# Kernel tuning notes

Measured on AMD Instinct MI355X. Metric: run time of the kernel, lower is better.

The kernel has to match this reference:

```python
import jax, jax.numpy as jnp
import numpy as np

N = 50000
E = 600000
D = 128
BN_EPS = 1e-5


def _gcn_layer(x, src, dst, ew, W, b, n):
    # x: [N, Din] -> [N, Dout]; PyG GCNConv: linear, symmetric norm (self-loops
    # already appended to src/dst/ew by caller), gather, scatter-add, bias.
    h = x @ W  # [N, Dout]
    deg = jax.ops.segment_sum(ew, dst, num_segments=n)  # [N]
    dinv = jnp.where(deg > 0, jax.lax.rsqrt(jnp.maximum(deg, 1e-30)), 0.0)
    norm = dinv[src] * ew * dinv[dst]  # [E+N]
    msg = h[src] * norm[:, None]  # [E+N, Dout] -- dominant memory traffic
    out = jax.ops.segment_sum(msg, dst, num_segments=n)
    return out + b


def _bn_eval(x, gamma, beta, mean, var):
    return (x - mean) * jax.lax.rsqrt(var + BN_EPS) * gamma + beta


def setup_inputs() -> dict:
    key = jax.random.key(0)
    ks = jax.random.split(key, 16)
    s = 1.0 / np.sqrt(D)
    inp = {
        "x": jax.random.normal(ks[0], (N, D), dtype=jnp.float32),
        "edge_index": jax.random.randint(ks[1], (2, E), 0, N, dtype=jnp.int32),
        "edge_weight": jax.random.uniform(ks[2], (E,), dtype=jnp.float32),
        "W0": jax.random.uniform(ks[3], (D, D), jnp.float32, -s, s),
        "b0": jnp.zeros((D,), jnp.float32),
        "W1": jax.random.uniform(ks[4], (D, D), jnp.float32, -s, s),
        "b1": jnp.zeros((D,), jnp.float32),
        "gamma0": jnp.ones((D,), jnp.float32),
        "beta0": jnp.zeros((D,), jnp.float32),
        "mean0": 0.1 * jax.random.normal(ks[5], (D,), jnp.float32),
        "var0": jax.random.uniform(ks[6], (D,), jnp.float32, 0.5, 1.5),
        "gamma1": jnp.ones((D,), jnp.float32),
        "beta1": jnp.zeros((D,), jnp.float32),
        "mean1": 0.1 * jax.random.normal(ks[7], (D,), jnp.float32),
        "var1": jax.random.uniform(ks[8], (D,), jnp.float32, 0.5, 1.5),
        "act_params": jnp.ones((2,), jnp.float32),  # activation_params init = ones(num_layers)
    }
    return inp


def reference(x, edge_index, edge_weight, W0, b0, W1, b1, gamma0, beta0, mean0, var0, gamma1, beta1, mean1, var1, act_params):
    # Add self-loops with weight 1 (PyG gcn_norm fill_value=1), shared by both layers.
    loop = jnp.arange(N, dtype=edge_index.dtype)
    src = jnp.concatenate([edge_index[0], loop])
    dst = jnp.concatenate([edge_index[1], loop])
    ew = jnp.concatenate([edge_weight, jnp.ones((N,), edge_weight.dtype)])

    # layer 0: conv -> BN (eval: running stats) -> adaptive ReLU/GELU blend
    h = _gcn_layer(x, src, dst, ew, W0, b0, N)
    h = _bn_eval(h, gamma0, beta0, mean0, var0)
    alpha = jax.nn.sigmoid(act_params[0])
    h = alpha * jax.nn.relu(h) + (1.0 - alpha) * jax.nn.gelu(h, approximate=False)
    # dropout: identity in eval mode

    # layer 1 (last): conv -> BN, no activation/dropout
    h = _gcn_layer(h, src, dst, ew, W1, b1, N)
    h = _bn_eval(h, gamma1, beta1, mean1, var1)
    return h
```

## Files before the change

kernel.cpp:

```cpp
#include <hip/hip_runtime.h>
#include <hip/hip_fp16.h>
#include <math.h>
#include <type_traits>

#define D 128
#define BN_EPS 1e-5f

typedef _Float16 half8 __attribute__((ext_vector_type(8)));
typedef float f32x4 __attribute__((ext_vector_type(4)));

__global__ void k_zero4(uint4* p, int n4) {
  int i = blockIdx.x * blockDim.x + threadIdx.x;
  if (i < n4) p[i] = make_uint4(0u, 0u, 0u, 0u);
}

__global__ void k_cnt_rank(const int* __restrict__ dst, int* cnt16,
                           int* __restrict__ rank, int e) {
  int i = blockIdx.x * blockDim.x + threadIdx.x;
  if (i < e) rank[i] = atomicAdd(&cnt16[(size_t)dst[i] * 16], 1);
}

__global__ __launch_bounds__(1024) void k_scan1(const int* __restrict__ cnt16,
                                                int* __restrict__ off, int* bsum, int n) {
  __shared__ int ws[16];
  const int tid = threadIdx.x;
  const int i = blockIdx.x * 1024 + tid;
  int v = (i < n) ? cnt16[(size_t)i * 16] : 0;
  int x = v;
#pragma unroll
  for (int d = 1; d < 64; d <<= 1) {
    int y = __shfl_up(x, d, 64);
    if ((tid & 63) >= d) x += y;
  }
  const int wid = tid >> 6;
  if ((tid & 63) == 63) ws[wid] = x;
  __syncthreads();
  if (wid == 0) {
    int s = (tid < 16) ? ws[tid] : 0;
#pragma unroll
    for (int d = 1; d < 16; d <<= 1) {
      int y = __shfl_up(s, d, 64);
      if (tid >= d && tid < 16) s += y;
    }
    if (tid < 16) ws[tid] = s;
  }
  __syncthreads();
  int woff = (wid > 0) ? ws[wid - 1] : 0;
  if (i < n) off[i] = woff + x - v;
  if (tid == 1023) bsum[blockIdx.x] = ws[15];
}

__global__ __launch_bounds__(1024) void k_scan2(int* bsum, int nb, int* total_loc) {
  __shared__ int ws[16];
  const int tid = threadIdx.x;
  int v = (tid < nb) ? bsum[tid] : 0;
  int x = v;
#pragma unroll
  for (int d = 1; d < 64; d <<= 1) {
    int y = __shfl_up(x, d, 64);
    if ((tid & 63) >= d) x += y;
  }
  const int wid = tid >> 6;
  if ((tid & 63) == 63) ws[wid] = x;
  __syncthreads();
  if (wid == 0) {
    int s = (tid < 16) ? ws[tid] : 0;
#pragma unroll
    for (int d = 1; d < 16; d <<= 1) {
      int y = __shfl_up(s, d, 64);
      if (tid >= d && tid < 16) s += y;
    }
    if (tid < 16) ws[tid] = s;
  }
  __syncthreads();
  int woff = (wid > 0) ? ws[wid - 1] : 0;
  if (tid < nb) bsum[tid] = woff + x - v;
  if (tid == 1023) *total_loc = ws[15];
}

__global__ __launch_bounds__(1024) void k_scan3(int* off, const int* __restrict__ bsum, int n) {
  const int i = blockIdx.x * 1024 + threadIdx.x;
  if (i < n) off[i] += bsum[blockIdx.x];
}

__global__ void k_bucket(const int* __restrict__ src, const int* __restrict__ dst,
                         const float* __restrict__ ew, const int* __restrict__ off,
                         const int* __restrict__ rank, uint2* __restrict__ pack, int e) {
  int i = blockIdx.x * blockDim.x + threadIdx.x;
  if (i < e) {
    int d = dst[i];
    int pos = off[d] + rank[i];
    pack[pos] = make_uint2((unsigned)src[i], __float_as_uint(ew[i]));
  }
}

__global__ void k_degdinv(const int* __restrict__ off, const uint2* __restrict__ pack,
                          float* __restrict__ dinv, int n) {
  int g = blockIdx.x * blockDim.x + threadIdx.x;
  if (g < n) {
    float deg = 1.0f;
    int k1 = off[g + 1];
    for (int k = off[g]; k < k1; ++k) deg += __uint_as_float(pack[k].y);
    dinv[g] = rsqrtf(deg);
  }
}

__global__ void k_packW(const float* __restrict__ W0, const float* __restrict__ W1,
                        _Float16* __restrict__ p0, _Float16* __restrict__ p1) {
  const float* W = blockIdx.x ? W1 : W0;
  _Float16* P = blockIdx.x ? p1 : p0;
  for (int idx = threadIdx.x; idx < 32 * 64; idx += 256) {
    int ntks = idx >> 6;
    int lane = idx & 63;
    int nt = ntks >> 2, ks = ntks & 3;
    int kb = ks * 32 + (lane >> 4) * 8;
    int c = nt * 16 + (lane & 15);
#pragma unroll
    for (int i = 0; i < 8; ++i)
      P[(size_t)idx * 8 + i] = (_Float16)W[(size_t)(kb + i) * D + c];
  }
}

template <typename T>
__global__ __launch_bounds__(256) void k_gemm_mfma(const T* __restrict__ X,
                                                   const _Float16* __restrict__ Bp,
                                                   __half* __restrict__ H, int n) {
  const int lane = threadIdx.x & 63;
  const int wave = threadIdx.x >> 6;
  const int r0 = blockIdx.x * 64 + wave * 16;
  const int arow = r0 + (lane & 15);
  const int kbase = (lane >> 4) * 8;
  const bool av = arow < n;

  f32x4 acc[8];
#pragma unroll
  for (int t = 0; t < 8; ++t) acc[t] = (f32x4){0.f, 0.f, 0.f, 0.f};

#pragma unroll
  for (int ks = 0; ks < 4; ++ks) {
    half8 a;
    if (av) {
      if constexpr (std::is_same<T, float>::value) {
        const float* ap = X + (size_t)arow * D + ks * 32 + kbase;
        float4 f0 = *(const float4*)ap;
        float4 f1 = *(const float4*)(ap + 4);
        a[0] = (_Float16)f0.x; a[1] = (_Float16)f0.y;
        a[2] = (_Float16)f0.z; a[3] = (_Float16)f0.w;
        a[4] = (_Float16)f1.x; a[5] = (_Float16)f1.y;
        a[6] = (_Float16)f1.z; a[7] = (_Float16)f1.w;
      } else {
        a = *(const half8*)((const __half*)X + (size_t)arow * D + ks * 32 + kbase);
      }
    } else {
#pragma unroll
      for (int i = 0; i < 8; ++i) a[i] = (_Float16)0.f;
    }
#pragma unroll
    for (int nt = 0; nt < 8; ++nt) {
      half8 b = *(const half8*)(Bp + ((size_t)(nt * 4 + ks) * 64 + lane) * 8);
      acc[nt] = __builtin_amdgcn_mfma_f32_16x16x32_f16(a, b, acc[nt], 0, 0, 0);
    }
  }

  const int rbase = (lane >> 4) * 4;
  const int col = lane & 15;
#pragma unroll
  for (int nt = 0; nt < 8; ++nt) {
#pragma unroll
    for (int j = 0; j < 4; ++j) {
      int rr = r0 + rbase + j;
      if (rr < n) H[(size_t)rr * D + nt * 16 + col] = __float2half(acc[nt][j]);
    }
  }
}

__device__ __forceinline__ void h8_to_f(const uint4& r, float* f) {
  const __half2* hp = (const __half2*)&r;
#pragma unroll
  for (int t = 0; t < 4; ++t) {
    float2 v = __half22float2(hp[t]);
    f[2 * t] = v.x; f[2 * t + 1] = v.y;
  }
}

template <typename OutT, bool ACT>
__global__ __launch_bounds__(256) void k_agg(const __half* __restrict__ H,
                                             const int* __restrict__ off,
                                             const uint2* __restrict__ pack,
                                             const float* __restrict__ dinv,
                                             const float* __restrict__ bias,
                                             const float* __restrict__ gamma,
                                             const float* __restrict__ beta,
                                             const float* __restrict__ mean,
                                             const float* __restrict__ var,
                                             const float* __restrict__ act_params,
                                             OutT* __restrict__ out, int n) {
  int g = blockIdx.x * 16 + (threadIdx.x >> 4);
  if (g >= n) return;
  const int j = (threadIdx.x & 15) * 8;

  float acc[8];
#pragma unroll
  for (int t = 0; t < 8; ++t) acc[t] = 0.f;

  int k = off[g], k1 = off[g + 1];
  for (; k + 3 < k1; k += 4) {
    uint2 p0 = pack[k], p1 = pack[k + 1], p2 = pack[k + 2], p3 = pack[k + 3];
    float w0 = dinv[p0.x] * __uint_as_float(p0.y);
    float w1 = dinv[p1.x] * __uint_as_float(p1.y);
    float w2 = dinv[p2.x] * __uint_as_float(p2.y);
    float w3 = dinv[p3.x] * __uint_as_float(p3.y);
    uint4 r0 = *(const uint4*)(H + (size_t)p0.x * D + j);
    uint4 r1 = *(const uint4*)(H + (size_t)p1.x * D + j);
    uint4 r2 = *(const uint4*)(H + (size_t)p2.x * D + j);
    uint4 r3 = *(const uint4*)(H + (size_t)p3.x * D + j);
    float f0[8], f1[8], f2[8], f3[8];
    h8_to_f(r0, f0); h8_to_f(r1, f1); h8_to_f(r2, f2); h8_to_f(r3, f3);
#pragma unroll
    for (int t = 0; t < 8; ++t)
      acc[t] += w0 * f0[t] + w1 * f1[t] + w2 * f2[t] + w3 * f3[t];
  }
  for (; k < k1; ++k) {
    uint2 p = pack[k];
    float w = dinv[p.x] * __uint_as_float(p.y);
    uint4 r = *(const uint4*)(H + (size_t)p.x * D + j);
    float f[8];
    h8_to_f(r, f);
#pragma unroll
    for (int t = 0; t < 8; ++t) acc[t] += w * f[t];
  }

  float dg = dinv[g];
  uint4 rs = *(const uint4*)(H + (size_t)g * D + j);
  float fs[8];
  h8_to_f(rs, fs);
#pragma unroll
  for (int t = 0; t < 8; ++t) acc[t] = dg * acc[t] + dg * dg * fs[t];

  float bb[8], gm[8], bt[8], mn[8], vr[8];
  *(float4*)&bb[0] = *(const float4*)(bias + j);  *(float4*)&bb[4] = *(const float4*)(bias + j + 4);
  *(float4*)&gm[0] = *(const float4*)(gamma + j); *(float4*)&gm[4] = *(const float4*)(gamma + j + 4);
  *(float4*)&bt[0] = *(const float4*)(beta + j);  *(float4*)&bt[4] = *(const float4*)(beta + j + 4);
  *(float4*)&mn[0] = *(const float4*)(mean + j);  *(float4*)&mn[4] = *(const float4*)(mean + j + 4);
  *(float4*)&vr[0] = *(const float4*)(var + j);   *(float4*)&vr[4] = *(const float4*)(var + j + 4);

  float alpha = ACT ? 1.f / (1.f + expf(-act_params[0])) : 0.f;

#pragma unroll
  for (int t = 0; t < 8; ++t) {
    float vv = (acc[t] + bb[t] - mn[t]) * rsqrtf(vr[t] + BN_EPS) * gm[t] + bt[t];
    if (ACT) {
      float rl = fmaxf(vv, 0.f);
      float ge = 0.5f * vv * (1.f + erff(vv * 0.70710678118654752f));
      vv = alpha * rl + (1.f - alpha) * ge;
    }
    acc[t] = vv;
  }
  if constexpr (std::is_same<OutT, __half>::value) {
    uint4 st;
    __half2* hp = (__half2*)&st;
    hp[0] = __floats2half2_rn(acc[0], acc[1]);
    hp[1] = __floats2half2_rn(acc[2], acc[3]);
    hp[2] = __floats2half2_rn(acc[4], acc[5]);
    hp[3] = __floats2half2_rn(acc[6], acc[7]);
    *(uint4*)(out + (size_t)g * D + j) = st;
  } else {
    *(float4*)(out + (size_t)g * D + j)     = make_float4(acc[0], acc[1], acc[2], acc[3]);
    *(float4*)(out + (size_t)g * D + j + 4) = make_float4(acc[4], acc[5], acc[6], acc[7]);
  }
}

extern "C" void kernel_launch(void* const* d_in, const int* in_sizes, int n_in,
                              void* d_out, int out_size, void* d_ws, size_t ws_size,
                              hipStream_t stream) {
  const float* x      = (const float*)d_in[0];
  const int*   ei     = (const int*)d_in[1];
  const float* ew     = (const float*)d_in[2];
  const float* W0     = (const float*)d_in[3];
  const float* b0     = (const float*)d_in[4];
  const float* W1     = (const float*)d_in[5];
  const float* b1     = (const float*)d_in[6];
  const float* gamma0 = (const float*)d_in[7];
  const float* beta0  = (const float*)d_in[8];
  const float* mean0  = (const float*)d_in[9];
  const float* var0   = (const float*)d_in[10];
  const float* gamma1 = (const float*)d_in[11];
  const float* beta1  = (const float*)d_in[12];
  const float* mean1  = (const float*)d_in[13];
  const float* var1   = (const float*)d_in[14];
  const float* act    = (const float*)d_in[15];

  const int n = in_sizes[0] / D;
  const int e = in_sizes[2];
  const int* srcp = ei;
  const int* dstp = ei + e;

  uintptr_t p = (uintptr_t)d_ws;
  auto carve = [&p](size_t bytes) -> void* {
    void* r = (void*)p;
    p += (bytes + 255) & ~(size_t)255;
    return r;
  };
  float*    dinv  = (float*)carve(sizeof(float) * n);
  int*      off   = (int*)carve(sizeof(int) * (n + 1));
  int*      rank  = (int*)carve(sizeof(int) * e);
  int*      bsum  = (int*)carve(sizeof(int) * 1024);
  int*      cnt16 = (int*)carve(sizeof(int) * (size_t)n * 16);
  _Float16* w0p   = (_Float16*)carve(sizeof(_Float16) * 32 * 64 * 8);
  _Float16* w1p   = (_Float16*)carve(sizeof(_Float16) * 32 * 64 * 8);
  uint2*    pack  = (uint2*)carve(sizeof(uint2) * e);
  __half*   h16   = (__half*)carve(sizeof(__half) * (size_t)n * D);
  __half*   a16   = (__half*)carve(sizeof(__half) * (size_t)n * D);
  float*    out   = (float*)d_out;

  const int tpb = 256;
  const int nb_n = (n + tpb - 1) / tpb;
  const int nb_e = (e + tpb - 1) / tpb;
  const int nb_s = (n + 1023) / 1024;
  const int Gg   = (n + 63) / 64;
  const int nz4  = n * 4;

  k_zero4<<<(nz4 + tpb - 1) / tpb, tpb, 0, stream>>>((uint4*)cnt16, nz4);
  k_packW<<<2, tpb, 0, stream>>>(W0, W1, w0p, w1p);
  k_cnt_rank<<<nb_e, tpb, 0, stream>>>(dstp, cnt16, rank, e);
  k_scan1<<<nb_s, 1024, 0, stream>>>(cnt16, off, bsum, n);
  k_scan2<<<1, 1024, 0, stream>>>(bsum, nb_s, off + n);
  k_scan3<<<nb_s, 1024, 0, stream>>>(off, bsum, n);
  k_bucket<<<nb_e, tpb, 0, stream>>>(srcp, dstp, ew, off, rank, pack, e);
  k_degdinv<<<nb_n, tpb, 0, stream>>>(off, pack, dinv, n);

  k_gemm_mfma<float><<<Gg, tpb, 0, stream>>>(x, w0p, h16, n);
  k_agg<__half, true><<<(n + 15) / 16, tpb, 0, stream>>>(
      h16, off, pack, dinv, b0, gamma0, beta0, mean0, var0, act, a16, n);

  k_gemm_mfma<__half><<<Gg, tpb, 0, stream>>>(a16, w1p, h16, n);
  k_agg<float, false><<<(n + 15) / 16, tpb, 0, stream>>>(
      h16, off, pack, dinv, b1, gamma1, beta1, mean1, var1, act, out, n);
}
```

Before: 146.1 us.

## Fuse preprocessing kernels and layer-0 aggregation with layer-1 GEMM

Merges zeroing and weight packing into one launch, and runs the edge-count atomics in the same launch as the first GEMM using block-index partitioning. The two scan tail kernels become one, with each block re-scanning the block sums in a single wavefront. The layer-0 aggregation now writes its activated rows into shared memory and immediately multiplies them by W1 with MFMA. This removes the intermediate half-precision activation buffer round trip and several kernel launches. The trade-offs are more shared memory per block, a block barrier inside the aggregation, and a scan that assumes at most 64 scan blocks.

```diff
diff --git a/kernel.cpp b/kernel.cpp
--- a/kernel.cpp
+++ b/kernel.cpp
@@ -9,15 +9,87 @@
 typedef _Float16 half8 __attribute__((ext_vector_type(8)));
 typedef float f32x4 __attribute__((ext_vector_type(4)));
 
-__global__ void k_zero4(uint4* p, int n4) {
-  int i = blockIdx.x * blockDim.x + threadIdx.x;
-  if (i < n4) p[i] = make_uint4(0u, 0u, 0u, 0u);
-}
-
-__global__ void k_cnt_rank(const int* __restrict__ dst, int* cnt16,
-                           int* __restrict__ rank, int e) {
-  int i = blockIdx.x * blockDim.x + threadIdx.x;
-  if (i < e) rank[i] = atomicAdd(&cnt16[(size_t)dst[i] * 16], 1);
+__global__ void k_init(uint4* __restrict__ z, int n4,
+                       const float* __restrict__ W0, const float* __restrict__ W1,
+                       _Float16* __restrict__ p0, _Float16* __restrict__ p1, int Z) {
+  if ((int)blockIdx.x < Z) {
+    int i = blockIdx.x * 256 + threadIdx.x;
+    if (i < n4) z[i] = make_uint4(0u, 0u, 0u, 0u);
+    return;
+  }
+  const float* W = (blockIdx.x - Z) ? W1 : W0;
+  _Float16* P = (blockIdx.x - Z) ? p1 : p0;
+  for (int idx = threadIdx.x; idx < 32 * 64; idx += 256) {
+    int ntks = idx >> 6;
+    int lane = idx & 63;
+    int nt = ntks >> 2, ks = ntks & 3;
+    int kb = ks * 32 + (lane >> 4) * 8;
+    int c = nt * 16 + (lane & 15);
+#pragma unroll
+    for (int i = 0; i < 8; ++i)
+      P[(size_t)idx * 8 + i] = (_Float16)W[(size_t)(kb + i) * D + c];
+  }
+}
+
+__global__ __launch_bounds__(256) void k_cnt_gemm0(const float* __restrict__ X,
+                                                   const _Float16* __restrict__ Bp,
+                                                   __half* __restrict__ H,
+                                                   const int* __restrict__ dst,
+                                                   int* cnt16, int* __restrict__ rank,
+                                                   int n, int e, int Gc) {
+  if ((int)blockIdx.x < Gc) {
+    int base = blockIdx.x * 1024 + threadIdx.x;
+#pragma unroll
+    for (int jj = 0; jj < 4; ++jj) {
+      int i = base + jj * 256;
+      if (i < e) rank[i] = atomicAdd(&cnt16[(size_t)dst[i] * 16], 1);
+    }
+    return;
+  }
+
+  const int lane = threadIdx.x & 63;
+  const int wave = threadIdx.x >> 6;
+  const int r0 = (blockIdx.x - Gc) * 64 + wave * 16;
+  const int arow = r0 + (lane & 15);
+  const int kbase = (lane >> 4) * 8;
+  const bool av = arow < n;
+
+  f32x4 acc[8];
+#pragma unroll
+  for (int t = 0; t < 8; ++t) acc[t] = (f32x4){0.f, 0.f, 0.f, 0.f};
+
+#pragma unroll
+  for (int ks = 0; ks < 4; ++ks) {
+    half8 a;
+    if (av) {
+      const float* ap = X + (size_t)arow * D + ks * 32 + kbase;
+      float4 f0 = *(const float4*)ap;
+      float4 f1 = *(const float4*)(ap + 4);
+      a[0] = (_Float16)f0.x; a[1] = (_Float16)f0.y;
+      a[2] = (_Float16)f0.z; a[3] = (_Float16)f0.w;
+      a[4] = (_Float16)f1.x; a[5] = (_Float16)f1.y;
+      a[6] = (_Float16)f1.z; a[7] = (_Float16)f1.w;
+    } else {
+#pragma unroll
+      for (int i = 0; i < 8; ++i) a[i] = (_Float16)0.f;
+    }
+#pragma unroll
+    for (int nt = 0; nt < 8; ++nt) {
+      half8 b = *(const half8*)(Bp + ((size_t)(nt * 4 + ks) * 64 + lane) * 8);
+      acc[nt] = __builtin_amdgcn_mfma_f32_16x16x32_f16(a, b, acc[nt], 0, 0, 0);
+    }
+  }
+
+  const int rbase = (lane >> 4) * 4;
+  const int col = lane & 15;
+#pragma unroll
+  for (int nt = 0; nt < 8; ++nt) {
+#pragma unroll
+    for (int j = 0; j < 4; ++j) {
+      int rr = r0 + rbase + j;
+      if (rr < n) H[(size_t)rr * D + nt * 16 + col] = __float2half(acc[nt][j]);
+    }
+  }
 }
 
 __global__ __launch_bounds__(1024) void k_scan1(const int* __restrict__ cnt16,
@@ -50,37 +122,25 @@
   if (tid == 1023) bsum[blockIdx.x] = ws[15];
 }
 
-__global__ __launch_bounds__(1024) void k_scan2(int* bsum, int nb, int* total_loc) {
-  __shared__ int ws[16];
+__global__ __launch_bounds__(1024) void k_scan23(int* off, const int* __restrict__ bsum,
+                                                 int n, int nb) {
+  __shared__ int sh[2];
   const int tid = threadIdx.x;
-  int v = (tid < nb) ? bsum[tid] : 0;
-  int x = v;
-#pragma unroll
-  for (int d = 1; d < 64; d <<= 1) {
-    int y = __shfl_up(x, d, 64);
-    if ((tid & 63) >= d) x += y;
-  }
-  const int wid = tid >> 6;
-  if ((tid & 63) == 63) ws[wid] = x;
+  if (tid < 64) {
+    int x = (tid < nb) ? bsum[tid] : 0;
+#pragma unroll
+    for (int d = 1; d < 64; d <<= 1) {
+      int y = __shfl_up(x, d, 64);
+      if (tid >= d) x += y;
+    }
+    int pfx = (blockIdx.x > 0) ? __shfl(x, (int)blockIdx.x - 1, 64) : 0;
+    int tot = __shfl(x, nb - 1, 64);
+    if (tid == 0) { sh[0] = pfx; sh[1] = tot; }
+  }
   __syncthreads();
-  if (wid == 0) {
-    int s = (tid < 16) ? ws[tid] : 0;
-#pragma unroll
-    for (int d = 1; d < 16; d <<= 1) {
-      int y = __shfl_up(s, d, 64);
-      if (tid >= d && tid < 16) s += y;
-    }
-    if (tid < 16) ws[tid] = s;
-  }
-  __syncthreads();
-  int woff = (wid > 0) ? ws[wid - 1] : 0;
-  if (tid < nb) bsum[tid] = woff + x - v;
-  if (tid == 1023) *total_loc = ws[15];
-}
-
-__global__ __launch_bounds__(1024) void k_scan3(int* off, const int* __restrict__ bsum, int n) {
-  const int i = blockIdx.x * 1024 + threadIdx.x;
-  if (i < n) off[i] += bsum[blockIdx.x];
+  const int i = blockIdx.x * 1024 + tid;
+  if (i < n) off[i] += sh[0];
+  if (blockIdx.x == 0 && tid == 0) off[n] = sh[1];
 }
 
 __global__ void k_bucket(const int* __restrict__ src, const int* __restrict__ dst,
@@ -105,81 +165,149 @@
   }
 }
 
-__global__ void k_packW(const float* __restrict__ W0, const float* __restrict__ W1,
-                        _Float16* __restrict__ p0, _Float16* __restrict__ p1) {
-  const float* W = blockIdx.x ? W1 : W0;
-  _Float16* P = blockIdx.x ? p1 : p0;
-  for (int idx = threadIdx.x; idx < 32 * 64; idx += 256) {
-    int ntks = idx >> 6;
-    int lane = idx & 63;
-    int nt = ntks >> 2, ks = ntks & 3;
-    int kb = ks * 32 + (lane >> 4) * 8;
-    int c = nt * 16 + (lane & 15);
-#pragma unroll
-    for (int i = 0; i < 8; ++i)
-      P[(size_t)idx * 8 + i] = (_Float16)W[(size_t)(kb + i) * D + c];
-  }
-}
-
-template <typename T>
-__global__ __launch_bounds__(256) void k_gemm_mfma(const T* __restrict__ X,
-                                                   const _Float16* __restrict__ Bp,
-                                                   __half* __restrict__ H, int n) {
-  const int lane = threadIdx.x & 63;
-  const int wave = threadIdx.x >> 6;
-  const int r0 = blockIdx.x * 64 + wave * 16;
-  const int arow = r0 + (lane & 15);
-  const int kbase = (lane >> 4) * 8;
-  const bool av = arow < n;
-
-  f32x4 acc[8];
-#pragma unroll
-  for (int t = 0; t < 8; ++t) acc[t] = (f32x4){0.f, 0.f, 0.f, 0.f};
-
-#pragma unroll
-  for (int ks = 0; ks < 4; ++ks) {
-    half8 a;
-    if (av) {
-      if constexpr (std::is_same<T, float>::value) {
-        const float* ap = X + (size_t)arow * D + ks * 32 + kbase;
-        float4 f0 = *(const float4*)ap;
-        float4 f1 = *(const float4*)(ap + 4);
-        a[0] = (_Float16)f0.x; a[1] = (_Float16)f0.y;
-        a[2] = (_Float16)f0.z; a[3] = (_Float16)f0.w;
-        a[4] = (_Float16)f1.x; a[5] = (_Float16)f1.y;
-        a[6] = (_Float16)f1.z; a[7] = (_Float16)f1.w;
-      } else {
-        a = *(const half8*)((const __half*)X + (size_t)arow * D + ks * 32 + kbase);
-      }
-    } else {
-#pragma unroll
-      for (int i = 0; i < 8; ++i) a[i] = (_Float16)0.f;
-    }
-#pragma unroll
-    for (int nt = 0; nt < 8; ++nt) {
-      half8 b = *(const half8*)(Bp + ((size_t)(nt * 4 + ks) * 64 + lane) * 8);
-      acc[nt] = __builtin_amdgcn_mfma_f32_16x16x32_f16(a, b, acc[nt], 0, 0, 0);
-    }
-  }
-
-  const int rbase = (lane >> 4) * 4;
-  const int col = lane & 15;
-#pragma unroll
-  for (int nt = 0; nt < 8; ++nt) {
-#pragma unroll
-    for (int j = 0; j < 4; ++j) {
-      int rr = r0 + rbase + j;
-      if (rr < n) H[(size_t)rr * D + nt * 16 + col] = __float2half(acc[nt][j]);
-    }
-  }
-}
-
 __device__ __forceinline__ void h8_to_f(const uint4& r, float* f) {
   const __half2* hp = (const __half2*)&r;
 #pragma unroll
   for (int t = 0; t < 4; ++t) {
     float2 v = __half22float2(hp[t]);
     f[2 * t] = v.x; f[2 * t + 1] = v.y;
+  }
+}
+
+template <bool ACT>
+__device__ __forceinline__ void agg_node(const __half* __restrict__ H,
+                                         const int* __restrict__ off,
+                                         const uint2* __restrict__ pack,
+                                         const float* __restrict__ dinv,
+                                         const float* __restrict__ bias,
+                                         const float* __restrict__ gamma,
+                                         const float* __restrict__ beta,
+                                         const float* __restrict__ mean,
+                                         const float* __restrict__ var,
+                                         float alpha, int g, int j, float* acc) {
+#pragma unroll
+  for (int t = 0; t < 8; ++t) acc[t] = 0.f;
+
+  int k = off[g], k1 = off[g + 1];
+  for (; k + 3 < k1; k += 4) {
+    uint2 p0 = pack[k], p1 = pack[k + 1], p2 = pack[k + 2], p3 = pack[k + 3];
+    float w0 = dinv[p0.x] * __uint_as_float(p0.y);
+    float w1 = dinv[p1.x] * __uint_as_float(p1.y);
+    float w2 = dinv[p2.x] * __uint_as_float(p2.y);
+    float w3 = dinv[p3.x] * __uint_as_float(p3.y);
+    uint4 r0 = *(const uint4*)(H + (size_t)p0.x * D + j);
+    uint4 r1 = *(const uint4*)(H + (size_t)p1.x * D + j);
+    uint4 r2 = *(const uint4*)(H + (size_t)p2.x * D + j);
+    uint4 r3 = *(const uint4*)(H + (size_t)p3.x * D + j);
+    float f0[8], f1[8], f2[8], f3[8];
+    h8_to_f(r0, f0); h8_to_f(r1, f1); h8_to_f(r2, f2); h8_to_f(r3, f3);
+#pragma unroll
+    for (int t = 0; t < 8; ++t)
+      acc[t] += w0 * f0[t] + w1 * f1[t] + w2 * f2[t] + w3 * f3[t];
+  }
+  for (; k < k1; ++k) {
+    uint2 p = pack[k];
+    float w = dinv[p.x] * __uint_as_float(p.y);
+    uint4 r = *(const uint4*)(H + (size_t)p.x * D + j);
+    float f[8];
+    h8_to_f(r, f);
+#pragma unroll
+    for (int t = 0; t < 8; ++t) acc[t] += w * f[t];
+  }
+
+  float dg = dinv[g];
+  uint4 rs = *(const uint4*)(H + (size_t)g * D + j);
+  float fs[8];
+  h8_to_f(rs, fs);
+#pragma unroll
+  for (int t = 0; t < 8; ++t) acc[t] = dg * acc[t] + dg * dg * fs[t];
+
+  float bb[8], gm[8], bt[8], mn[8], vr[8];
+  *(float4*)&bb[0] = *(const float4*)(bias + j);  *(float4*)&bb[4] = *(const float4*)(bias + j + 4);
+  *(float4*)&gm[0] = *(const float4*)(gamma + j); *(float4*)&gm[4] = *(const float4*)(gamma + j + 4);
+  *(float4*)&bt[0] = *(const float4*)(beta + j);  *(float4*)&bt[4] = *(const float4*)(beta + j + 4);
+  *(float4*)&mn[0] = *(const float4*)(mean + j);  *(float4*)&mn[4] = *(const float4*)(mean + j + 4);
+  *(float4*)&vr[0] = *(const float4*)(var + j);   *(float4*)&vr[4] = *(const float4*)(var + j + 4);
+
+#pragma unroll
+  for (int t = 0; t < 8; ++t) {
+    float vv = (acc[t] + bb[t] - mn[t]) * rsqrtf(vr[t] + BN_EPS) * gm[t] + bt[t];
+    if (ACT) {
+      float rl = fmaxf(vv, 0.f);
+      float ge = 0.5f * vv * (1.f + erff(vv * 0.70710678118654752f));
+      vv = alpha * rl + (1.f - alpha) * ge;
+    }
+    acc[t] = vv;
+  }
+}
+
+__global__ __launch_bounds__(256) void k_agg_gemm(const __half* __restrict__ H,
+                                                  const int* __restrict__ off,
+                                                  const uint2* __restrict__ pack,
+                                                  const float* __restrict__ dinv,
+                                                  const float* __restrict__ bias,
+                                                  const float* __restrict__ gamma,
+                                                  const float* __restrict__ beta,
+                                                  const float* __restrict__ mean,
+                                                  const float* __restrict__ var,
+                                                  const float* __restrict__ act_params,
+                                                  const _Float16* __restrict__ Bp,
+                                                  __half* __restrict__ Hout, int n) {
+  __shared__ _Float16 sA[32][136];
+  const int tid = threadIdx.x;
+  const int row0 = blockIdx.x * 32;
+  const int grp = tid >> 4;
+  const int j = (tid & 15) * 8;
+  const float alpha = 1.f / (1.f + expf(-act_params[0]));
+
+#pragma unroll
+  for (int it = 0; it < 2; ++it) {
+    int lr = it * 16 + grp;
+    int g = row0 + lr;
+    half8 st;
+    if (g < n) {
+      float acc[8];
+      agg_node<true>(H, off, pack, dinv, bias, gamma, beta, mean, var, alpha, g, j, acc);
+#pragma unroll
+      for (int t = 0; t < 8; ++t) st[t] = (_Float16)acc[t];
+    } else {
+#pragma unroll
+      for (int t = 0; t < 8; ++t) st[t] = (_Float16)0.f;
+    }
+    *(half8*)&sA[lr][j] = st;
+  }
+  __syncthreads();
+
+  const int lane = tid & 63;
+  const int wave = tid >> 6;
+  const int lrow = (wave & 1) * 16;
+  const int ntb = (wave >> 1) * 4;
+  const int arowl = lrow + (lane & 15);
+  const int kbase = (lane >> 4) * 8;
+
+  f32x4 acc[4];
+#pragma unroll
+  for (int t = 0; t < 4; ++t) acc[t] = (f32x4){0.f, 0.f, 0.f, 0.f};
+
+#pragma unroll
+  for (int ks = 0; ks < 4; ++ks) {
+    half8 a = *(const half8*)&sA[arowl][ks * 32 + kbase];
+#pragma unroll
+    for (int nt = 0; nt < 4; ++nt) {
+      half8 b = *(const half8*)(Bp + ((size_t)((ntb + nt) * 4 + ks) * 64 + lane) * 8);
+      acc[nt] = __builtin_amdgcn_mfma_f32_16x16x32_f16(a, b, acc[nt], 0, 0, 0);
+    }
+  }
+
+  const int rbase = (lane >> 4) * 4;
+  const int col = lane & 15;
+#pragma unroll
+  for (int nt = 0; nt < 4; ++nt) {
+#pragma unroll
+    for (int jj = 0; jj < 4; ++jj) {
+      int rr = row0 + lrow + rbase + jj;
+      if (rr < n) Hout[(size_t)rr * D + (ntb + nt) * 16 + col] = __float2half(acc[nt][jj]);
+    }
   }
 }
 
@@ -198,64 +326,11 @@
   int g = blockIdx.x * 16 + (threadIdx.x >> 4);
   if (g >= n) return;
   const int j = (threadIdx.x & 15) * 8;
+  const float alpha = ACT ? 1.f / (1.f + expf(-act_params[0])) : 0.f;
 
   float acc[8];
-#pragma unroll
-  for (int t = 0; t < 8; ++t) acc[t] = 0.f;
-
-  int k = off[g], k1 = off[g + 1];
-  for (; k + 3 < k1; k += 4) {
-    uint2 p0 = pack[k], p1 = pack[k + 1], p2 = pack[k + 2], p3 = pack[k + 3];
-    float w0 = dinv[p0.x] * __uint_as_float(p0.y);
-    float w1 = dinv[p1.x] * __uint_as_float(p1.y);
-    float w2 = dinv[p2.x] * __uint_as_float(p2.y);
-    float w3 = dinv[p3.x] * __uint_as_float(p3.y);
-    uint4 r0 = *(const uint4*)(H + (size_t)p0.x * D + j);
-    uint4 r1 = *(const uint4*)(H + (size_t)p1.x * D + j);
-    uint4 r2 = *(const uint4*)(H + (size_t)p2.x * D + j);
-    uint4 r3 = *(const uint4*)(H + (size_t)p3.x * D + j);
-    float f0[8], f1[8], f2[8], f3[8];
-    h8_to_f(r0, f0); h8_to_f(r1, f1); h8_to_f(r2, f2); h8_to_f(r3, f3);
-#pragma unroll
-    for (int t = 0; t < 8; ++t)
-      acc[t] += w0 * f0[t] + w1 * f1[t] + w2 * f2[t] + w3 * f3[t];
-  }
-  for (; k < k1; ++k) {
-    uint2 p = pack[k];
-    float w = dinv[p.x] * __uint_as_float(p.y);
-    uint4 r = *(const uint4*)(H + (size_t)p.x * D + j);
-    float f[8];
-    h8_to_f(r, f);
-#pragma unroll
-    for (int t = 0; t < 8; ++t) acc[t] += w * f[t];
-  }
-
-  float dg = dinv[g];
-  uint4 rs = *(const uint4*)(H + (size_t)g * D + j);
-  float fs[8];
-  h8_to_f(rs, fs);
-#pragma unroll
-  for (int t = 0; t < 8; ++t) acc[t] = dg * acc[t] + dg * dg * fs[t];
-
-  float bb[8], gm[8], bt[8], mn[8], vr[8];
-  *(float4*)&bb[0] = *(const float4*)(bias + j);  *(float4*)&bb[4] = *(const float4*)(bias + j + 4);
-  *(float4*)&gm[0] = *(const float4*)(gamma + j); *(float4*)&gm[4] = *(const float4*)(gamma + j + 4);
-  *(float4*)&bt[0] = *(const float4*)(beta + j);  *(float4*)&bt[4] = *(const float4*)(beta + j + 4);
-  *(float4*)&mn[0] = *(const float4*)(mean + j);  *(float4*)&mn[4] = *(const float4*)(mean + j + 4);
-  *(float4*)&vr[0] = *(const float4*)(var + j);   *(float4*)&vr[4] = *(const float4*)(var + j + 4);
-
-  float alpha = ACT ? 1.f / (1.f + expf(-act_params[0])) : 0.f;
-
-#pragma unroll
-  for (int t = 0; t < 8; ++t) {
-    float vv = (acc[t] + bb[t] - mn[t]) * rsqrtf(vr[t] + BN_EPS) * gm[t] + bt[t];
-    if (ACT) {
-      float rl = fmaxf(vv, 0.f);
-      float ge = 0.5f * vv * (1.f + erff(vv * 0.70710678118654752f));
-      vv = alpha * rl + (1.f - alpha) * ge;
-    }
-    acc[t] = vv;
-  }
+  agg_node<ACT>(H, off, pack, dinv, bias, gamma, beta, mean, var, alpha, g, j, acc);
+
   if constexpr (std::is_same<OutT, __half>::value) {
     uint4 st;
     __half2* hp = (__half2*)&st;
@@ -310,30 +385,28 @@
   _Float16* w1p   = (_Float16*)carve(sizeof(_Float16) * 32 * 64 * 8);
   uint2*    pack  = (uint2*)carve(sizeof(uint2) * e);
   __half*   h16   = (__half*)carve(sizeof(__half) * (size_t)n * D);
-  __half*   a16   = (__half*)carve(sizeof(__half) * (size_t)n * D);
+  __half*   h16b  = (__half*)carve(sizeof(__half) * (size_t)n * D);
   float*    out   = (float*)d_out;
 
   const int tpb = 256;
   const int nb_n = (n + tpb - 1) / tpb;
   const int nb_e = (e + tpb - 1) / tpb;
   const int nb_s = (n + 1023) / 1024;
+  const int Gc   = (e + 1023) / 1024;
   const int Gg   = (n + 63) / 64;
   const int nz4  = n * 4;
-
-  k_zero4<<<(nz4 + tpb - 1) / tpb, tpb, 0, stream>>>((uint4*)cnt16, nz4);
-  k_packW<<<2, tpb, 0, stream>>>(W0, W1, w0p, w1p);
-  k_cnt_rank<<<nb_e, tpb, 0, stream>>>(dstp, cnt16, rank, e);
+  const int Z    = (nz4 + tpb - 1) / tpb;
+
+  k_init<<<Z + 2, tpb, 0, stream>>>((uint4*)cnt16, nz4, W0, W1, w0p, w1p, Z);
+  k_cnt_gemm0<<<Gc + Gg, tpb, 0, stream>>>(x, w0p, h16, dstp, cnt16, rank, n, e, Gc);
   k_scan1<<<nb_s, 1024, 0, stream>>>(cnt16, off, bsum, n);
-  k_scan2<<<1, 1024, 0, stream>>>(bsum, nb_s, off + n);
-  k_scan3<<<nb_s, 1024, 0, stream>>>(off, bsum, n);
+  k_scan23<<<nb_s, 1024, 0, stream>>>(off, bsum, n, nb_s);
   k_bucket<<<nb_e, tpb, 0, stream>>>(srcp, dstp, ew, off, rank, pack, e);
   k_degdinv<<<nb_n, tpb, 0, stream>>>(off, pack, dinv, n);
 
-  k_gemm_mfma<float><<<Gg, tpb, 0, stream>>>(x, w0p, h16, n);
-  k_agg<__half, true><<<(n + 15) / 16, tpb, 0, stream>>>(
-      h16, off, pack, dinv, b0, gamma0, beta0, mean0, var0, act, a16, n);
-
-  k_gemm_mfma<__half><<<Gg, tpb, 0, stream>>>(a16, w1p, h16, n);
+  k_agg_gemm<<<(n + 31) / 32, tpb, 0, stream>>>(
+      h16, off, pack, dinv, b0, gamma0, beta0, mean0, var0, act, w1p, h16b, n);
+
   k_agg<float, false><<<(n + 15) / 16, tpb, 0, stream>>>(
-      h16, off, pack, dinv, b1, gamma1, beta1, mean1, var1, act, out, n);
-}
+      h16b, off, pack, dinv, b1, gamma1, beta1, mean1, var1, act, out, n);
+}
```

After: 129.5 us. 1.13x faster.
